# Performance work log

Hardware: AMD Instinct MI355X
Metric: run time of the kernel (lower is better)

Reference implementation:

```python
import jax, jax.numpy as jnp
import numpy as np

GROUP_SIZE = 128


def _dequant_weight(qweight, scales, qzeros, group_size=GROUP_SIZE):
    # qweight: [K//2, N] int, packed nibbles; scales: [K//g, N] fp16; qzeros: [K//2g, N] int
    low = (qweight & 15).astype(jnp.float16)
    high = ((qweight >> 4) & 15).astype(jnp.float16)
    K2, N = qweight.shape
    # interleave even rows = low nibble, odd rows = high nibble -> [K, N]
    w_q = jnp.stack([low, high], axis=1).reshape(2 * K2, N)
    zlow = (qzeros & 15).astype(jnp.float16)
    zhigh = ((qzeros >> 4) & 15).astype(jnp.float16)
    G2, _ = qzeros.shape
    zeros = jnp.stack([zlow, zhigh], axis=1).reshape(2 * G2, N)  # [K//g, N]
    scales_exp = jnp.repeat(scales, group_size, axis=0)          # [K, N]
    zeros_exp = jnp.repeat(zeros, group_size, axis=0)            # [K, N]
    return (w_q - zeros_exp) * scales_exp


def setup_inputs() -> dict:
    key = jax.random.key(0)
    k1, k2, k3, k4 = jax.random.split(key, 4)
    B, S, K, N = 4, 2048, 4096, 11008
    x = jax.random.normal(k1, (B, S, K), dtype=jnp.float16)
    qweight = jax.random.randint(k2, (K // 2, N), 0, 127, dtype=jnp.int32)
    scales = jax.random.uniform(k3, (K // GROUP_SIZE, N), dtype=jnp.float16, minval=0.001, maxval=0.02)
    qzeros = jax.random.randint(k4, (K // GROUP_SIZE // 2, N), 0, 127, dtype=jnp.int32)
    return {"x": x, "qweight": qweight, "scales": scales, "qzeros": qzeros}


def reference(x, qweight, scales, qzeros):
    W = _dequant_weight(qweight, scales, qzeros)  # [K, N] fp16
    return jnp.matmul(x, W)  # [B, S, N]
```

## Files before the change

kernel.cpp:

```cpp
#include <hip/hip_runtime.h>
#include <cstdint>
#include <cstddef>
#include <type_traits>


typedef __bf16 bf16x8 __attribute__((ext_vector_type(8)));
typedef _Float16 halfx8 __attribute__((ext_vector_type(8)));
typedef _Float16 h2 __attribute__((ext_vector_type(2)));
typedef float floatx4 __attribute__((ext_vector_type(4)));
struct u4 { unsigned x, y, z, w; };

#define M_DIM 8192
#define K_DIM 4096
#define N_DIM 11008
#define BM 256
#define BN 128
#define BK 32

__device__ __forceinline__ unsigned short f2bf(float f) {
  unsigned u = __float_as_uint(f);
  return (unsigned short)((u + 0x7FFFu + ((u >> 16) & 1u)) >> 16);
}
__device__ __forceinline__ float bf2f(unsigned s) { return __uint_as_float(s << 16); }
__device__ __forceinline__ unsigned short f2h(float f) {
  _Float16 h = (_Float16)f;
  return __builtin_bit_cast(unsigned short, h);
}
__device__ __forceinline__ unsigned cvt_pk_bf16(float lo, float hi) {
  unsigned r;
  asm("v_cvt_pk_bf16_f32 %0, %1, %2" : "=v"(r) : "v"(lo), "v"(hi));
  return r;
}

__global__ void dtype_probe(const unsigned* __restrict__ sd, int* __restrict__ flag) {
  const unsigned lo = sd[threadIdx.x] & 0xFFFFu;
  const int is_bf = (lo >= 0x3A00u) && (lo < 0x3D00u);
  const int is_h  = (lo >= 0x1400u) && (lo < 0x2600u);
  const int f = __all(is_bf) ? 0 : (__all(is_h) ? 2 : 1);
  flag[0] = f;
}

template <int DT>
__launch_bounds__(512, 4)
__global__ void int4gemm_kernel(const void* __restrict__ xv,
                                const int* __restrict__ qw,
                                const void* __restrict__ sv,
                                const int* __restrict__ qz,
                                void* __restrict__ outv,
                                const int* __restrict__ flag) {
  if (*flag != DT) return;

  __shared__ __align__(16) unsigned short As[BM * BK];
  __shared__ __align__(16) unsigned Bs[BN * 16];
  __shared__ unsigned tbl[(DT == 1) ? (64 * BN) : (32 * BN)];

  const int t = threadIdx.x;
  const int m0 = blockIdx.x * BM;
  const int n0 = blockIdx.y * BN;

  for (int i = t; i < 32 * BN; i += 512) {
    const int g = i >> 7, j = i & (BN - 1);
    const int n = n0 + j;
    const int zp = qz[(size_t)(g >> 1) * N_DIM + n];
    const int z = (zp >> ((g & 1) * 4)) & 15;
    if constexpr (DT == 2) {
      const unsigned sb = ((const unsigned short*)sv)[(size_t)g * N_DIM + n];
      tbl[i] = sb | ((unsigned)f2h(1024.0f + (float)z) << 16);
    } else if constexpr (DT == 0) {
      const unsigned sb = ((const unsigned short*)sv)[(size_t)g * N_DIM + n];
      tbl[i] = sb | ((unsigned)z << 16);
    } else {
      tbl[i] = __float_as_uint(8388608.0f + (float)z);
      tbl[32 * BN + i] = ((const unsigned*)sv)[(size_t)g * N_DIM + n];
    }
  }

  const int lane = t & 63;
  const int wid = t >> 6;
  const int wm = (wid >> 1) * 64;
  const int wn = (wid & 1) * 64;
  const int lrow = lane & 15, lq = lane >> 4;
  const int xs = (lrow >> 1) & 3;
  const int aoff = ((lq ^ xs) << 3);
  const int boff = ((lq ^ xs) << 2);

  const int bn = t & 127;
  const int bh = t >> 7;
  const int bphys = ((bh ^ ((bn >> 1) & 3)) << 2);

  const int arow = t >> 2;
  const int acol = (((t & 3) ^ ((arow >> 1) & 3)) << 3);
  const unsigned short* xb = (const unsigned short*)xv;
  const unsigned short* ga0 = xb + (size_t)(m0 + arow) * K_DIM + acol;
  const unsigned short* ga1 = ga0 + (size_t)128 * K_DIM;
  char* lA0 = (char*)As + (wid << 10);
  char* lA1 = lA0 + 8192;

  const int* qp = qw + (size_t)4 * bh * N_DIM + n0 + bn;

  floatx4 acc[4][4];
#pragma unroll
  for (int mi = 0; mi < 4; ++mi)
#pragma unroll
    for (int ni = 0; ni < 4; ++ni) {
      acc[mi][ni][0] = 0.0f; acc[mi][ni][1] = 0.0f;
      acc[mi][ni][2] = 0.0f; acc[mi][ni][3] = 0.0f;
    }

  __syncthreads();

#pragma unroll 1
  for (int kt = 0; kt < K_DIM / BK; ++kt) {
    const int k0 = kt * BK;
    const int g = k0 >> 7;

    int p[4];
#pragma unroll
    for (int r = 0; r < 4; ++r) p[r] = qp[(size_t)r * N_DIM];

    if constexpr (DT != 1) {
      __builtin_amdgcn_global_load_lds(
          (const __attribute__((address_space(1))) unsigned*)(ga0 + k0),
          (__attribute__((address_space(3))) unsigned*)lA0, 16, 0, 0);
      __builtin_amdgcn_global_load_lds(
          (const __attribute__((address_space(1))) unsigned*)(ga1 + k0),
          (__attribute__((address_space(3))) unsigned*)lA1, 16, 0, 0);
    } else {
      const float* xf = (const float*)xv;
      const float* gf0 = xf + (size_t)(m0 + arow) * K_DIM + k0 + acol;
      const float* gf1 = gf0 + (size_t)128 * K_DIM;
      floatx4 fa = *(const floatx4*)gf0, fb = *(const floatx4*)(gf0 + 4);
      floatx4 fc = *(const floatx4*)gf1, fd = *(const floatx4*)(gf1 + 4);
      u4 p0v, p1v;
      p0v.x = cvt_pk_bf16(fa[0], fa[1]); p0v.y = cvt_pk_bf16(fa[2], fa[3]);
      p0v.z = cvt_pk_bf16(fb[0], fb[1]); p0v.w = cvt_pk_bf16(fb[2], fb[3]);
      p1v.x = cvt_pk_bf16(fc[0], fc[1]); p1v.y = cvt_pk_bf16(fc[2], fc[3]);
      p1v.z = cvt_pk_bf16(fd[0], fd[1]); p1v.w = cvt_pk_bf16(fd[2], fd[3]);
      *reinterpret_cast<u4*>((char*)As + t * 16) = p0v;
      *reinterpret_cast<u4*>((char*)As + t * 16 + 8192) = p1v;
    }

    const unsigned ts = tbl[(g << 7) + bn];
    u4 wv;
    if constexpr (DT == 2) {
      const unsigned s2 = __builtin_amdgcn_perm(ts, ts, 0x01000100u);
      const unsigned z2 = __builtin_amdgcn_perm(ts, ts, 0x03020302u);
      const h2 zh = __builtin_bit_cast(h2, z2);
      const h2 sh = __builtin_bit_cast(h2, s2);
      unsigned wpk[4];
#pragma unroll
      for (int r = 0; r < 4; ++r) {
        const unsigned P = (unsigned)p[r];
        const unsigned q2 = ((P & 15u) | ((P << 12) & 0xF0000u)) | 0x64006400u;
        const h2 w = (__builtin_bit_cast(h2, q2) - zh) * sh;
        wpk[r] = __builtin_bit_cast(unsigned, w);
      }
      wv.x = wpk[0]; wv.y = wpk[1]; wv.z = wpk[2]; wv.w = wpk[3];
    } else {
      float s, zo;
      if constexpr (DT == 0) {
        s = __uint_as_float(ts << 16);
        zo = __uint_as_float(0x4B000000u | (ts >> 16));
      } else {
        zo = __uint_as_float(ts);
        s = __uint_as_float(tbl[32 * BN + (g << 7) + bn]);
      }
      unsigned wpk[4];
#pragma unroll
      for (int r = 0; r < 4; ++r) {
        const unsigned P = (unsigned)p[r];
        const float fl = (__uint_as_float((P & 15u) | 0x4B000000u) - zo) * s;
        const float fh = (__uint_as_float(((P >> 4) & 15u) | 0x4B000000u) - zo) * s;
        wpk[r] = cvt_pk_bf16(fl, fh);
      }
      wv.x = wpk[0]; wv.y = wpk[1]; wv.z = wpk[2]; wv.w = wpk[3];
    }
    *reinterpret_cast<u4*>(&Bs[bn * 16 + bphys]) = wv;

    __syncthreads();

    using vecT = typename std::conditional<DT == 2, halfx8, bf16x8>::type;
    vecT av[4], bv[4];
#pragma unroll
    for (int mi = 0; mi < 4; ++mi)
      av[mi] = *reinterpret_cast<const vecT*>(&As[(wm + mi * 16 + lrow) * BK + aoff]);
#pragma unroll
    for (int ni = 0; ni < 4; ++ni)
      bv[ni] = *reinterpret_cast<const vecT*>(&Bs[(wn + ni * 16 + lrow) * 16 + boff]);
#pragma unroll
    for (int mi = 0; mi < 4; ++mi)
#pragma unroll
      for (int ni = 0; ni < 4; ++ni) {
        if constexpr (DT == 2)
          acc[mi][ni] = __builtin_amdgcn_mfma_f32_16x16x32_f16(av[mi], bv[ni],
                                                               acc[mi][ni], 0, 0, 0);
        else
          acc[mi][ni] = __builtin_amdgcn_mfma_f32_16x16x32_bf16(av[mi], bv[ni],
                                                                acc[mi][ni], 0, 0, 0);
      }
    __syncthreads();

    qp += (size_t)(BK / 2) * N_DIM;
  }

#pragma unroll
  for (int mi = 0; mi < 4; ++mi) {
#pragma unroll
    for (int rr = 0; rr < 4; ++rr) {
      const size_t rowoff = (size_t)(m0 + wm + mi * 16 + lq * 4 + rr) * N_DIM;
#pragma unroll
      for (int ni = 0; ni < 4; ++ni) {
        const size_t idx = rowoff + n0 + wn + ni * 16 + lrow;
        const float v = acc[mi][ni][rr];
        if constexpr (DT == 0)
          ((unsigned short*)outv)[idx] = f2bf(v);
        else if constexpr (DT == 1)
          ((float*)outv)[idx] = v;
        else
          ((unsigned short*)outv)[idx] = f2h(v);
      }
    }
  }
}

extern "C" void kernel_launch(void* const* d_in, const int* in_sizes, int n_in,
                              void* d_out, int out_size, void* d_ws, size_t ws_size,
                              hipStream_t stream) {
  const void* x = d_in[0];
  const int* qw = (const int*)d_in[1];
  const void* sc = d_in[2];
  const int* qz = (const int*)d_in[3];
  int* flag = (int*)d_ws;

  dtype_probe<<<1, 64, 0, stream>>>((const unsigned*)sc, flag);

  dim3 grid(M_DIM / BM, N_DIM / BN);
  int4gemm_kernel<0><<<grid, dim3(512), 0, stream>>>(x, qw, sc, qz, d_out, flag);
  int4gemm_kernel<1><<<grid, dim3(512), 0, stream>>>(x, qw, sc, qz, d_out, flag);
  int4gemm_kernel<2><<<grid, dim3(512), 0, stream>>>(x, qw, sc, qz, d_out, flag);
}
```

Baseline: 1.471 ms.

## Double-buffer LDS tiles and prefetch next K-step while computing current

Introduces ping-pong LDS buffers for A and dequantized B so the global loads and dequantization of the next K-step overlap the MFMA work on the current one, leaving one barrier per step instead of two. The per-block scale/zero table preload is removed; scales and zeros are now fetched from global memory one group ahead, inside the loop. For fp16/bf16 inputs the async global_load_lds path is replaced by register-staged loads followed by LDS stores, which raises register pressure and may cut occupancy under the 512x4 launch bounds.

Measured after the change: 1.922 ms. 30.7% more time.

```diff
diff --git a/kernel.cpp b/kernel.cpp
--- a/kernel.cpp
+++ b/kernel.cpp
@@ -16,6 +16,7 @@
 #define BM 256
 #define BN 128
 #define BK 32
+#define NG 32
 
 __device__ __forceinline__ unsigned short f2bf(float f) {
   unsigned u = __float_as_uint(f);
@@ -30,6 +31,48 @@
   unsigned r;
   asm("v_cvt_pk_bf16_f32 %0, %1, %2" : "=v"(r) : "v"(lo), "v"(hi));
   return r;
+}
+
+template <int DT>
+__device__ __forceinline__ u4 dq4(const int* p, float s, unsigned zob,
+                                  unsigned s2w, unsigned z2w) {
+  u4 wv;
+  if constexpr (DT == 2) {
+    const h2 zh = __builtin_bit_cast(h2, z2w);
+    const h2 sh = __builtin_bit_cast(h2, s2w);
+    unsigned w[4];
+#pragma unroll
+    for (int r = 0; r < 4; ++r) {
+      const unsigned P = (unsigned)p[r];
+      const unsigned q2 = ((P & 15u) | ((P << 12) & 0xF0000u)) | 0x64006400u;
+      const h2 t = (__builtin_bit_cast(h2, q2) - zh) * sh;
+      w[r] = __builtin_bit_cast(unsigned, t);
+    }
+    wv.x = w[0]; wv.y = w[1]; wv.z = w[2]; wv.w = w[3];
+  } else {
+    const float zo = __uint_as_float(zob);
+    unsigned w[4];
+#pragma unroll
+    for (int r = 0; r < 4; ++r) {
+      const unsigned P = (unsigned)p[r];
+      const float fl = (__uint_as_float((P & 15u) | 0x4B000000u) - zo) * s;
+      const float fh = (__uint_as_float(((P >> 4) & 15u) | 0x4B000000u) - zo) * s;
+      w[r] = cvt_pk_bf16(fl, fh);
+    }
+    wv.x = w[0]; wv.y = w[1]; wv.z = w[2]; wv.w = w[3];
+  }
+  return wv;
+}
+
+__device__ __forceinline__ void packA(void* dst0, void* dst1, floatx4 fa,
+                                      floatx4 fb, floatx4 fc, floatx4 fd) {
+  u4 w0, w1;
+  w0.x = cvt_pk_bf16(fa[0], fa[1]); w0.y = cvt_pk_bf16(fa[2], fa[3]);
+  w0.z = cvt_pk_bf16(fb[0], fb[1]); w0.w = cvt_pk_bf16(fb[2], fb[3]);
+  w1.x = cvt_pk_bf16(fc[0], fc[1]); w1.y = cvt_pk_bf16(fc[2], fc[3]);
+  w1.z = cvt_pk_bf16(fd[0], fd[1]); w1.w = cvt_pk_bf16(fd[2], fd[3]);
+  *reinterpret_cast<u4*>(dst0) = w0;
+  *reinterpret_cast<u4*>(dst1) = w1;
 }
 
 __global__ void dtype_probe(const unsigned* __restrict__ sd, int* __restrict__ flag) {
@@ -50,30 +93,12 @@
                                 const int* __restrict__ flag) {
   if (*flag != DT) return;
 
-  __shared__ __align__(16) unsigned short As[BM * BK];
-  __shared__ __align__(16) unsigned Bs[BN * 16];
-  __shared__ unsigned tbl[(DT == 1) ? (64 * BN) : (32 * BN)];
+  __shared__ __align__(16) unsigned short As[2][BM * BK];
+  __shared__ __align__(16) unsigned Bs[2][BN * 16];
 
   const int t = threadIdx.x;
   const int m0 = blockIdx.x * BM;
   const int n0 = blockIdx.y * BN;
-
-  for (int i = t; i < 32 * BN; i += 512) {
-    const int g = i >> 7, j = i & (BN - 1);
-    const int n = n0 + j;
-    const int zp = qz[(size_t)(g >> 1) * N_DIM + n];
-    const int z = (zp >> ((g & 1) * 4)) & 15;
-    if constexpr (DT == 2) {
-      const unsigned sb = ((const unsigned short*)sv)[(size_t)g * N_DIM + n];
-      tbl[i] = sb | ((unsigned)f2h(1024.0f + (float)z) << 16);
-    } else if constexpr (DT == 0) {
-      const unsigned sb = ((const unsigned short*)sv)[(size_t)g * N_DIM + n];
-      tbl[i] = sb | ((unsigned)z << 16);
-    } else {
-      tbl[i] = __float_as_uint(8388608.0f + (float)z);
-      tbl[32 * BN + i] = ((const unsigned*)sv)[(size_t)g * N_DIM + n];
-    }
-  }
 
   const int lane = t & 63;
   const int wid = t >> 6;
@@ -86,17 +111,17 @@
 
   const int bn = t & 127;
   const int bh = t >> 7;
-  const int bphys = ((bh ^ ((bn >> 1) & 3)) << 2);
+  const int bsw = bn * 16 + ((bh ^ ((bn >> 1) & 3)) << 2);
+  const int ncol = n0 + bn;
 
   const int arow = t >> 2;
   const int acol = (((t & 3) ^ ((arow >> 1) & 3)) << 3);
-  const unsigned short* xb = (const unsigned short*)xv;
-  const unsigned short* ga0 = xb + (size_t)(m0 + arow) * K_DIM + acol;
-  const unsigned short* ga1 = ga0 + (size_t)128 * K_DIM;
-  char* lA0 = (char*)As + (wid << 10);
-  char* lA1 = lA0 + 8192;
-
-  const int* qp = qw + (size_t)4 * bh * N_DIM + n0 + bn;
+  const size_t rstep = (size_t)128 * K_DIM;
+  const float* gAf = (const float*)xv + (size_t)(m0 + arow) * K_DIM + acol;
+  const unsigned short* gAh =
+      (const unsigned short*)xv + (size_t)(m0 + arow) * K_DIM + acol;
+
+  const int* qp = qw + (size_t)(4 * bh) * N_DIM + ncol;
 
   floatx4 acc[4][4];
 #pragma unroll
@@ -107,100 +132,140 @@
       acc[mi][ni][2] = 0.0f; acc[mi][ni][3] = 0.0f;
     }
 
+  float s_cur = 0.f; unsigned zo_cur = 0, s2_cur = 0, z2_cur = 0;
+  {
+    const int zp0 = qz[ncol];
+    const int z0 = zp0 & 15;
+    if constexpr (DT == 1) {
+      s_cur = ((const float*)sv)[ncol];
+      zo_cur = 0x4B000000u | (unsigned)z0;
+    } else if constexpr (DT == 0) {
+      s_cur = bf2f(((const unsigned short*)sv)[ncol]);
+      zo_cur = 0x4B000000u | (unsigned)z0;
+    } else {
+      const unsigned sb = ((const unsigned short*)sv)[ncol];
+      s2_cur = sb | (sb << 16);
+      z2_cur = 0x64006400u | (unsigned)z0 | ((unsigned)z0 << 16);
+    }
+  }
+
+  {
+    int p0[4];
+#pragma unroll
+    for (int r = 0; r < 4; ++r) p0[r] = qp[(size_t)r * N_DIM];
+    if constexpr (DT == 1) {
+      floatx4 fa = *(const floatx4*)(gAf);
+      floatx4 fb = *(const floatx4*)(gAf + 4);
+      floatx4 fc = *(const floatx4*)(gAf + rstep);
+      floatx4 fd = *(const floatx4*)(gAf + rstep + 4);
+      packA((char*)As[0] + t * 16, (char*)As[0] + t * 16 + 8192, fa, fb, fc, fd);
+    } else {
+      const u4 a0 = *(const u4*)(gAh);
+      const u4 a1 = *(const u4*)(gAh + rstep);
+      *reinterpret_cast<u4*>((char*)As[0] + t * 16) = a0;
+      *reinterpret_cast<u4*>((char*)As[0] + t * 16 + 8192) = a1;
+    }
+    const u4 wv = dq4<DT>(p0, s_cur, zo_cur, s2_cur, z2_cur);
+    *reinterpret_cast<u4*>(&Bs[0][bsw]) = wv;
+  }
+  gAf += BK; gAh += BK;
+  qp += (size_t)16 * N_DIM;
   __syncthreads();
 
+  using vecT = typename std::conditional<DT == 2, halfx8, bf16x8>::type;
+
 #pragma unroll 1
-  for (int kt = 0; kt < K_DIM / BK; ++kt) {
-    const int k0 = kt * BK;
-    const int g = k0 >> 7;
-
-    int p[4];
-#pragma unroll
-    for (int r = 0; r < 4; ++r) p[r] = qp[(size_t)r * N_DIM];
-
-    if constexpr (DT != 1) {
-      __builtin_amdgcn_global_load_lds(
-          (const __attribute__((address_space(1))) unsigned*)(ga0 + k0),
-          (__attribute__((address_space(3))) unsigned*)lA0, 16, 0, 0);
-      __builtin_amdgcn_global_load_lds(
-          (const __attribute__((address_space(1))) unsigned*)(ga1 + k0),
-          (__attribute__((address_space(3))) unsigned*)lA1, 16, 0, 0);
-    } else {
-      const float* xf = (const float*)xv;
-      const float* gf0 = xf + (size_t)(m0 + arow) * K_DIM + k0 + acol;
-      const float* gf1 = gf0 + (size_t)128 * K_DIM;
-      floatx4 fa = *(const floatx4*)gf0, fb = *(const floatx4*)(gf0 + 4);
-      floatx4 fc = *(const floatx4*)gf1, fd = *(const floatx4*)(gf1 + 4);
-      u4 p0v, p1v;
-      p0v.x = cvt_pk_bf16(fa[0], fa[1]); p0v.y = cvt_pk_bf16(fa[2], fa[3]);
-      p0v.z = cvt_pk_bf16(fb[0], fb[1]); p0v.w = cvt_pk_bf16(fb[2], fb[3]);
-      p1v.x = cvt_pk_bf16(fc[0], fc[1]); p1v.y = cvt_pk_bf16(fc[2], fc[3]);
-      p1v.z = cvt_pk_bf16(fd[0], fd[1]); p1v.w = cvt_pk_bf16(fd[2], fd[3]);
-      *reinterpret_cast<u4*>((char*)As + t * 16) = p0v;
-      *reinterpret_cast<u4*>((char*)As + t * 16 + 8192) = p1v;
-    }
-
-    const unsigned ts = tbl[(g << 7) + bn];
-    u4 wv;
-    if constexpr (DT == 2) {
-      const unsigned s2 = __builtin_amdgcn_perm(ts, ts, 0x01000100u);
-      const unsigned z2 = __builtin_amdgcn_perm(ts, ts, 0x03020302u);
-      const h2 zh = __builtin_bit_cast(h2, z2);
-      const h2 sh = __builtin_bit_cast(h2, s2);
-      unsigned wpk[4];
-#pragma unroll
-      for (int r = 0; r < 4; ++r) {
-        const unsigned P = (unsigned)p[r];
-        const unsigned q2 = ((P & 15u) | ((P << 12) & 0xF0000u)) | 0x64006400u;
-        const h2 w = (__builtin_bit_cast(h2, q2) - zh) * sh;
-        wpk[r] = __builtin_bit_cast(unsigned, w);
-      }
-      wv.x = wpk[0]; wv.y = wpk[1]; wv.z = wpk[2]; wv.w = wpk[3];
-    } else {
-      float s, zo;
-      if constexpr (DT == 0) {
-        s = __uint_as_float(ts << 16);
-        zo = __uint_as_float(0x4B000000u | (ts >> 16));
-      } else {
-        zo = __uint_as_float(ts);
-        s = __uint_as_float(tbl[32 * BN + (g << 7) + bn]);
-      }
-      unsigned wpk[4];
-#pragma unroll
-      for (int r = 0; r < 4; ++r) {
-        const unsigned P = (unsigned)p[r];
-        const float fl = (__uint_as_float((P & 15u) | 0x4B000000u) - zo) * s;
-        const float fh = (__uint_as_float(((P >> 4) & 15u) | 0x4B000000u) - zo) * s;
-        wpk[r] = cvt_pk_bf16(fl, fh);
-      }
-      wv.x = wpk[0]; wv.y = wpk[1]; wv.z = wpk[2]; wv.w = wpk[3];
-    }
-    *reinterpret_cast<u4*>(&Bs[bn * 16 + bphys]) = wv;
-
-    __syncthreads();
-
-    using vecT = typename std::conditional<DT == 2, halfx8, bf16x8>::type;
-    vecT av[4], bv[4];
-#pragma unroll
-    for (int mi = 0; mi < 4; ++mi)
-      av[mi] = *reinterpret_cast<const vecT*>(&As[(wm + mi * 16 + lrow) * BK + aoff]);
-#pragma unroll
-    for (int ni = 0; ni < 4; ++ni)
-      bv[ni] = *reinterpret_cast<const vecT*>(&Bs[(wn + ni * 16 + lrow) * 16 + boff]);
-#pragma unroll
-    for (int mi = 0; mi < 4; ++mi)
-#pragma unroll
-      for (int ni = 0; ni < 4; ++ni) {
-        if constexpr (DT == 2)
-          acc[mi][ni] = __builtin_amdgcn_mfma_f32_16x16x32_f16(av[mi], bv[ni],
-                                                               acc[mi][ni], 0, 0, 0);
+  for (int g = 0; g < NG; ++g) {
+    float sNf = 0.f; unsigned sNh = 0; int zpN = 0;
+    float s_nx = 0.f; unsigned zo_nx = 0, s2_nx = 0, z2_nx = 0;
+
+#pragma unroll
+    for (int kk = 0; kk < 4; ++kk) {
+      const int cur = kk & 1, nxt = cur ^ 1;
+      const bool stage = (g < NG - 1) || (kk < 3);
+
+      floatx4 fa{}, fb{}, fc{}, fd{};
+      u4 a0{}, a1{};
+      int pn[4] = {0, 0, 0, 0};
+      if (stage) {
+        if constexpr (DT == 1) {
+          fa = *(const floatx4*)(gAf);
+          fb = *(const floatx4*)(gAf + 4);
+          fc = *(const floatx4*)(gAf + rstep);
+          fd = *(const floatx4*)(gAf + rstep + 4);
+        } else {
+          a0 = *(const u4*)(gAh);
+          a1 = *(const u4*)(gAh + rstep);
+        }
+#pragma unroll
+        for (int r = 0; r < 4; ++r) pn[r] = qp[(size_t)r * N_DIM];
+      }
+      if (kk == 2) {
+        const int gn = (g < NG - 1) ? g + 1 : g;
+        if constexpr (DT == 1)
+          sNf = ((const float*)sv)[(size_t)gn * N_DIM + ncol];
         else
-          acc[mi][ni] = __builtin_amdgcn_mfma_f32_16x16x32_bf16(av[mi], bv[ni],
-                                                                acc[mi][ni], 0, 0, 0);
-      }
-    __syncthreads();
-
-    qp += (size_t)(BK / 2) * N_DIM;
+          sNh = ((const unsigned short*)sv)[(size_t)gn * N_DIM + ncol];
+        zpN = qz[(size_t)(gn >> 1) * N_DIM + ncol];
+      }
+
+      vecT av[4], bv[4];
+#pragma unroll
+      for (int mi = 0; mi < 4; ++mi)
+        av[mi] = *reinterpret_cast<const vecT*>(
+            &As[cur][(wm + mi * 16 + lrow) * BK + aoff]);
+#pragma unroll
+      for (int ni = 0; ni < 4; ++ni)
+        bv[ni] = *reinterpret_cast<const vecT*>(
+            &Bs[cur][(wn + ni * 16 + lrow) * 16 + boff]);
+
+      if (stage) {
+        if constexpr (DT == 1)
+          packA((char*)As[nxt] + t * 16, (char*)As[nxt] + t * 16 + 8192,
+                fa, fb, fc, fd);
+        else {
+          *reinterpret_cast<u4*>((char*)As[nxt] + t * 16) = a0;
+          *reinterpret_cast<u4*>((char*)As[nxt] + t * 16 + 8192) = a1;
+        }
+      }
+
+#pragma unroll
+      for (int mi = 0; mi < 4; ++mi)
+#pragma unroll
+        for (int ni = 0; ni < 4; ++ni) {
+          if constexpr (DT == 2)
+            acc[mi][ni] = __builtin_amdgcn_mfma_f32_16x16x32_f16(
+                av[mi], bv[ni], acc[mi][ni], 0, 0, 0);
+          else
+            acc[mi][ni] = __builtin_amdgcn_mfma_f32_16x16x32_bf16(
+                av[mi], bv[ni], acc[mi][ni], 0, 0, 0);
+        }
+
+      if (kk == 2) {
+        const int z = (zpN >> (((g + 1) & 1) * 4)) & 15;
+        if constexpr (DT == 1) {
+          s_nx = sNf; zo_nx = 0x4B000000u | (unsigned)z;
+        } else if constexpr (DT == 0) {
+          s_nx = bf2f(sNh); zo_nx = 0x4B000000u | (unsigned)z;
+        } else {
+          s2_nx = sNh | (sNh << 16);
+          z2_nx = 0x64006400u | (unsigned)z | ((unsigned)z << 16);
+        }
+      }
+      if (stage) {
+        u4 wv;
+        if (kk == 3)
+          wv = dq4<DT>(pn, s_nx, zo_nx, s2_nx, z2_nx);
+        else
+          wv = dq4<DT>(pn, s_cur, zo_cur, s2_cur, z2_cur);
+        *reinterpret_cast<u4*>(&Bs[nxt][bsw]) = wv;
+      }
+
+      gAf += BK; gAh += BK;
+      qp += (size_t)16 * N_DIM;
+      __syncthreads();
+    }
+    s_cur = s_nx; zo_cur = zo_nx; s2_cur = s2_nx; z2_cur = z2_nx;
   }
 
 #pragma unroll
```
